# Performance work log

Measured on AMD Instinct MI355X. Metric: run time of the kernel, lower is better.

The kernel has to match this reference:

```python
import jax, jax.numpy as jnp
import numpy as np

N_OFFSETS = 72            # number of y-rows a lane proposal is sampled at (LaneATT)
N_STRIPS = N_OFFSETS - 1  # 71
IMG_W = 640.0             # nominal image width for x coordinates


def setup_inputs() -> dict:
    key = jax.random.key(0)
    k1, k2 = jax.random.split(key)
    n = 8192
    raw = jax.random.uniform(k1, (n, 2 + 3 + N_OFFSETS), dtype=jnp.float32)
    # LaneATT proposal layout: [score0, score1, start_y, start_x, length, xs(72)]
    start_y = raw[:, 2]                      # normalized [0,1]
    start_x = raw[:, 3] * IMG_W
    length = raw[:, 4] * N_STRIPS            # length in strips
    xs = raw[:, 5:] * IMG_W                  # x coords in pixels
    proposals = jnp.concatenate(
        [raw[:, :2], start_y[:, None], start_x[:, None], length[:, None], xs], axis=1
    )
    scores = jax.random.uniform(k2, (n,), dtype=jnp.float32)
    return {"proposals": proposals, "scores": scores, "nms_thres": 50, "nms_topk": 8}


def _line_nms(proposals, scores, nms_thres, nms_topk):
    """Greedy line NMS over lane proposals (LaneATT semantics)."""
    n = proposals.shape[0]
    order = jnp.argsort(-scores)
    p = proposals[order]                                   # [n, 77] sorted by score desc
    starts = jnp.round(p[:, 2] * N_STRIPS).astype(jnp.int32)       # [n]
    ends = jnp.minimum(starts + jnp.round(p[:, 4]).astype(jnp.int32) - 1, N_STRIPS)
    xs = p[:, 5:]                                          # [n, 72]
    k_idx = jnp.arange(N_OFFSETS)
    thr = jnp.float32(nms_thres)

    # suppression matrix row-by-row via lax.map to bound peak memory
    def supp_row(args):
        xi, si, ei = args
        ps = jnp.maximum(si, starts)                       # [n] pairwise overlap start
        pe = jnp.minimum(ei, ends)                         # [n] pairwise overlap end
        valid = (k_idx[None, :] >= ps[:, None]) & (k_idx[None, :] <= pe[:, None])
        d = jnp.sum(jnp.where(valid, jnp.abs(xi[None, :] - xs), 0.0), axis=1)
        cnt = jnp.maximum(pe - ps + 1, 1).astype(jnp.float32)
        return (pe >= ps) & (d / cnt < thr)                # [n] bool

    S = jax.lax.map(supp_row, (xs, starts, ends))          # [n, n] bool

    # sequential greedy pass: keep highest-score lane, suppress its neighbors
    def step(removed, inp):
        s_row, i = inp
        alive = ~removed[i]
        removed = removed | (alive & s_row)
        return removed, alive

    _, keep = jax.lax.scan(step, jnp.zeros((n,), bool), (S, jnp.arange(n)))

    rank = jnp.cumsum(keep)
    sel = keep & (rank <= nms_topk)
    idx = jnp.where(sel, size=nms_topk, fill_value=n)[0]   # padded with n (zero row)
    p_pad = jnp.concatenate([p, jnp.zeros((1, p.shape[1]), p.dtype)], axis=0)
    s_pad = jnp.concatenate([scores[order], jnp.zeros((1,), scores.dtype)], axis=0)
    kept = jnp.concatenate([p_pad[idx], s_pad[idx][:, None]], axis=1)  # [topk, 78]
    num_kept = jnp.minimum(jnp.sum(keep), nms_topk)
    return kept, num_kept


def reference(proposals, scores, nms_thres, nms_topk):
    return _line_nms(proposals, scores, nms_thres, nms_topk)
```

## Files before the change

### kernel.cpp

```cpp
#include <hip/hip_runtime.h>


#define NTH    256
#define SLOTS  32
#define NWAVES (NTH / 64)
#define N_OFF  72
#define NSTRIP 71
#define PROW   77
#define MAXK   8

__device__ __forceinline__ unsigned long long pack_key(float s, int idx) {
    return ((unsigned long long)__float_as_uint(s) << 32) |
           (unsigned long long)(0xFFFFFFFFu - (unsigned)idx);
}
__device__ __forceinline__ int key_idx(unsigned long long k) {
    return (int)(0xFFFFFFFFu - (unsigned)(k & 0xFFFFFFFFu));
}

__global__ __launch_bounds__(NTH, 1) void lane_nms(
    const float* __restrict__ prop,
    const float* __restrict__ scores,
    const int* __restrict__ p_thres,
    const int* __restrict__ p_topk,
    float* __restrict__ out,
    int n, int out_rows)
{
    const int tid  = threadIdx.x;
    const int lane = tid & 63;
    const int wv   = tid >> 6;

    __shared__ unsigned long long s_wmax[NWAVES];
    __shared__ float s_buf[2][PROW + 1];
    __shared__ float s_kxs[MAXK][N_OFF];
    __shared__ int   s_ks[MAXK], s_ke[MAXK];
    __shared__ int   s_sup[2];

    const float thr = (float)(*p_thres);
    int topk = *p_topk;
    if (topk > out_rows) topk = out_rows;
    if (topk > MAXK)     topk = MAXK;

    unsigned long long key[SLOTS];
#pragma unroll
    for (int jo = 0; jo < SLOTS / 4; ++jo) {
        int base = jo * (NTH * 4) + tid * 4;
        if (base + 3 < n) {
            const float4 s4 = *reinterpret_cast<const float4*>(scores + base);
            key[jo * 4 + 0] = pack_key(s4.x, base + 0);
            key[jo * 4 + 1] = pack_key(s4.y, base + 1);
            key[jo * 4 + 2] = pack_key(s4.z, base + 2);
            key[jo * 4 + 3] = pack_key(s4.w, base + 3);
        } else {
#pragma unroll
            for (int c = 0; c < 4; ++c) {
                int idx = base + c;
                key[jo * 4 + c] = (idx < n) ? pack_key(scores[idx], idx) : 0ULL;
            }
        }
    }
    if (tid == 0) { s_sup[0] = 0; s_sup[1] = 0; }

    auto scan = [&](unsigned long long lim) {
        unsigned long long m = 0ULL;
#pragma unroll
        for (int j = 0; j < SLOTS; ++j) {
            unsigned long long k = key[j];
            if (k < lim && k > m) m = k;
        }
#pragma unroll
        for (int off = 32; off > 0; off >>= 1) {
            unsigned long long o = __shfl_down(m, off);
            if (o > m) m = o;
        }
        if (lane == 0) s_wmax[wv] = m;
    };
    auto merge = [&]() {
        unsigned long long m = s_wmax[0];
#pragma unroll
        for (int i = 1; i < NWAVES; ++i)
            if (s_wmax[i] > m) m = s_wmax[i];
        return m;
    };

    scan(~0ULL);
    __syncthreads();
    unsigned long long k1 = merge();
    __syncthreads();
    scan(k1);
    __syncthreads();
    unsigned long long k2 = merge();

    if (k1 != 0ULL) {
        int w = key_idx(k1);
        if (tid < PROW)       s_buf[0][tid]  = prop[(size_t)w * PROW + tid];
        else if (tid == PROW) s_buf[0][PROW] = scores[w];
    }
    if (k2 != 0ULL) {
        int w = key_idx(k2);
        if (tid >= NTH - PROW - 1) {
            int t = tid - (NTH - PROW - 1);
            s_buf[1][t] = (t < PROW) ? prop[(size_t)w * PROW + t] : scores[w];
        }
    }
    __syncthreads();

    int kept = 0, p = 0, q = 0;
    unsigned long long curk = k1, nxtk = k2;

    if (topk > 0) {
        while (curk != 0ULL) {
            scan(nxtk);
            float sy = s_buf[p][2];
            float ln = s_buf[p][4];
            int cs = (int)rintf(sy * (float)NSTRIP);
            int ce = cs + (int)rintf(ln) - 1;
            if (ce > NSTRIP) ce = NSTRIP;
            if (tid < kept) {
                int ps = cs > s_ks[tid] ? cs : s_ks[tid];
                int pe = ce < s_ke[tid] ? ce : s_ke[tid];
                if (pe >= ps) {
                    float d = 0.0f;
                    for (int k = ps; k <= pe; ++k)
                        d += fabsf(s_buf[p][5 + k] - s_kxs[tid][k]);
                    if (d / (float)(pe - ps + 1) < thr) s_sup[q] = 1;
                }
            }
            if (tid == NTH - 1) s_sup[q ^ 1] = 0;
            __syncthreads();

            unsigned long long k3 = merge();
            if (s_sup[q] == 0) {
                if (tid < PROW + 1) out[kept * (PROW + 1) + tid] = s_buf[p][tid];
                if (tid < N_OFF)    s_kxs[kept][tid] = s_buf[p][5 + tid];
                if (tid == 0) { s_ks[kept] = cs; s_ke[kept] = ce; }
                ++kept;
                if (kept >= topk) break;
            }
            __syncthreads();

            if (k3 != 0ULL) {
                int w = key_idx(k3);
                if (tid < PROW)       s_buf[p][tid]  = prop[(size_t)w * PROW + tid];
                else if (tid == PROW) s_buf[p][PROW] = scores[w];
            }
            curk = nxtk; nxtk = k3; p ^= 1; q ^= 1;
        }
    }

    for (int i = tid; i < (out_rows - kept) * (PROW + 1); i += NTH)
        out[kept * (PROW + 1) + i] = 0.0f;
    if (tid == 0) out[out_rows * (PROW + 1)] = (float)kept;
}

extern "C" void kernel_launch(void* const* d_in, const int* in_sizes, int n_in,
                              void* d_out, int out_size, void* d_ws, size_t ws_size,
                              hipStream_t stream) {
    const float* prop   = (const float*)d_in[0];
    const float* scores = (const float*)d_in[1];
    const int*   thres  = (const int*)d_in[2];
    const int*   topk   = (const int*)d_in[3];
    int n        = in_sizes[1];
    int out_rows = (out_size - 1) / (PROW + 1);
    lane_nms<<<1, NTH, 0, stream>>>(prop, scores, thres, topk,
                                    (float*)d_out, n, out_rows);
}
```

Before: 87.26 us.

## Select top candidates via bitonic threshold and run greedy NMS in one wave

Replaces the per-step block-wide argmax scan with a one-time selection. Each thread takes its local max, a 64-lane bitonic sort of the per-thread maxima yields a threshold, and keys at or above it go into a small sorted candidate list. The first rows are prefetched into shared memory and a single wave runs the greedy suppression over the candidates with ballots, so the loop needs no block barriers. If the candidates run out before topk lanes are kept, it falls back to the original scan loop resuming below the last candidate, which adds code and shared memory.

```diff
diff --git a/kernel.cpp b/kernel.cpp
--- a/kernel.cpp
+++ b/kernel.cpp
@@ -1,13 +1,15 @@
 #include <hip/hip_runtime.h>
 
 
-#define NTH    256
-#define SLOTS  32
-#define NWAVES (NTH / 64)
-#define N_OFF  72
-#define NSTRIP 71
-#define PROW   77
-#define MAXK   8
+#define NTH     256
+#define SLOTS   32
+#define NWAVES  (NTH / 64)
+#define N_OFF   72
+#define NSTRIP  71
+#define PROW    77
+#define MAXK    8
+#define CANDMAX 64
+#define PRE     16
 
 __device__ __forceinline__ unsigned long long pack_key(float s, int idx) {
     return ((unsigned long long)__float_as_uint(s) << 32) |
@@ -15,6 +17,24 @@
 }
 __device__ __forceinline__ int key_idx(unsigned long long k) {
     return (int)(0xFFFFFFFFu - (unsigned)(k & 0xFFFFFFFFu));
+}
+
+__device__ __forceinline__ unsigned long long bitonic64_desc(
+        unsigned long long v, int lane) {
+#pragma unroll
+    for (int k = 2; k <= 64; k <<= 1) {
+#pragma unroll
+        for (int j = k >> 1; j > 0; j >>= 1) {
+            unsigned long long pv = __shfl_xor(v, j);
+            bool lower   = (lane & j) == 0;
+            bool dirdesc = (lane & k) != 0;
+            bool keepmax = (dirdesc != lower);
+            unsigned long long mx = v > pv ? v : pv;
+            unsigned long long mn = v > pv ? pv : v;
+            v = keepmax ? mx : mn;
+        }
+    }
+    return v;
 }
 
 __global__ __launch_bounds__(NTH, 1) void lane_nms(
@@ -30,10 +50,16 @@
     const int wv   = tid >> 6;
 
     __shared__ unsigned long long s_wmax[NWAVES];
+    __shared__ unsigned long long s_tmax[NTH];
+    __shared__ unsigned long long s_cand[CANDMAX];
+    __shared__ unsigned long long s_thr64;
+    __shared__ unsigned long long s_resume;
+    __shared__ float s_rows[PRE][PROW + 1];
     __shared__ float s_buf[2][PROW + 1];
     __shared__ float s_kxs[MAXK][N_OFF];
     __shared__ int   s_ks[MAXK], s_ke[MAXK];
     __shared__ int   s_sup[2];
+    __shared__ int   s_cnt, s_kept, s_fb;
 
     const float thr = (float)(*p_thres);
     int topk = *p_topk;
@@ -58,56 +84,167 @@
             }
         }
     }
-    if (tid == 0) { s_sup[0] = 0; s_sup[1] = 0; }
-
-    auto scan = [&](unsigned long long lim) {
-        unsigned long long m = 0ULL;
-#pragma unroll
-        for (int j = 0; j < SLOTS; ++j) {
-            unsigned long long k = key[j];
-            if (k < lim && k > m) m = k;
-        }
-#pragma unroll
-        for (int off = 32; off > 0; off >>= 1) {
-            unsigned long long o = __shfl_down(m, off);
-            if (o > m) m = o;
-        }
-        if (lane == 0) s_wmax[wv] = m;
-    };
-    auto merge = [&]() {
-        unsigned long long m = s_wmax[0];
-#pragma unroll
-        for (int i = 1; i < NWAVES; ++i)
-            if (s_wmax[i] > m) m = s_wmax[i];
-        return m;
-    };
-
-    scan(~0ULL);
+    unsigned long long tmax = 0ULL;
+#pragma unroll
+    for (int j = 0; j < SLOTS; ++j)
+        if (key[j] > tmax) tmax = key[j];
+
+    s_tmax[tid] = tmax;
+    if (tid == 0) { s_cnt = 0; s_sup[0] = 0; s_sup[1] = 0; }
     __syncthreads();
-    unsigned long long k1 = merge();
+
+    if (wv == 0) {
+        unsigned long long g = s_tmax[lane * 4 + 0];
+        unsigned long long t1 = s_tmax[lane * 4 + 1]; if (t1 > g) g = t1;
+        unsigned long long t2 = s_tmax[lane * 4 + 2]; if (t2 > g) g = t2;
+        unsigned long long t3 = s_tmax[lane * 4 + 3]; if (t3 > g) g = t3;
+        g = bitonic64_desc(g, lane);
+        if (lane == 15) s_thr64 = g;
+    }
     __syncthreads();
-    scan(k1);
+    const unsigned long long T = s_thr64;
+
+#pragma unroll
+    for (int j = 0; j < SLOTS; ++j) {
+        unsigned long long k = key[j];
+        if (k != 0ULL && k >= T) {
+            int pos = atomicAdd(&s_cnt, 1);
+            if (pos < CANDMAX) s_cand[pos] = k;
+        }
+    }
     __syncthreads();
-    unsigned long long k2 = merge();
-
-    if (k1 != 0ULL) {
-        int w = key_idx(k1);
-        if (tid < PROW)       s_buf[0][tid]  = prop[(size_t)w * PROW + tid];
-        else if (tid == PROW) s_buf[0][PROW] = scores[w];
-    }
-    if (k2 != 0ULL) {
-        int w = key_idx(k2);
-        if (tid >= NTH - PROW - 1) {
-            int t = tid - (NTH - PROW - 1);
-            s_buf[1][t] = (t < PROW) ? prop[(size_t)w * PROW + t] : scores[w];
-        }
-    }
-    __syncthreads();
-
-    int kept = 0, p = 0, q = 0;
-    unsigned long long curk = k1, nxtk = k2;
-
-    if (topk > 0) {
+    const int  cnt  = s_cnt;
+    const bool fast = (cnt <= CANDMAX) && (topk > 0);
+
+    int kept = 0;
+    bool fb = (topk > 0);
+    unsigned long long resume = ~0ULL;
+
+    if (fast) {
+        const int ncand = cnt;
+        if (wv == 0) {
+            unsigned long long v = (lane < ncand) ? s_cand[lane] : 0ULL;
+            v = bitonic64_desc(v, lane);
+            s_cand[lane] = v;
+        }
+        __syncthreads();
+
+        const int npre = ncand < PRE ? ncand : PRE;
+        for (int i = tid; i < npre * (PROW + 1); i += NTH) {
+            int r = i / (PROW + 1), c = i - r * (PROW + 1);
+            int w = key_idx(s_cand[r]);
+            s_rows[r][c] = (c < PROW) ? prop[(size_t)w * PROW + c] : scores[w];
+        }
+        __syncthreads();
+
+        if (wv == 0) {
+            int  pref = npre;
+            int  k0 = 0;
+            bool hit_topk = false;
+            for (int c = 0; c < ncand; ++c) {
+                if (c >= pref) {
+                    int w = key_idx(s_cand[c]);
+                    for (int i = lane; i < PROW + 1; i += 64)
+                        s_rows[c & (PRE - 1)][i] =
+                            (i < PROW) ? prop[(size_t)w * PROW + i] : scores[w];
+                    asm volatile("s_waitcnt lgkmcnt(0)" ::: "memory");
+                    pref = c + 1;
+                }
+                const int slot = c & (PRE - 1);
+                float sy = s_rows[slot][2];
+                float ln = s_rows[slot][4];
+                int cs = (int)rintf(sy * (float)NSTRIP);
+                int ce = cs + (int)rintf(ln) - 1;
+                if (ce > NSTRIP) ce = NSTRIP;
+
+                bool pred = false;
+                {
+                    int j = lane >> 3, l = lane & 7;
+                    if (j < k0) {
+                        int ps = cs > s_ks[j] ? cs : s_ks[j];
+                        int pe = ce < s_ke[j] ? ce : s_ke[j];
+                        if (pe >= ps) {
+                            float d = 0.0f;
+                            for (int k = ps + l; k <= pe; k += 8)
+                                d += fabsf(s_rows[slot][5 + k] - s_kxs[j][k]);
+                            d += __shfl_down(d, 4, 8);
+                            d += __shfl_down(d, 2, 8);
+                            d += __shfl_down(d, 1, 8);
+                            if (l == 0 && d / (float)(pe - ps + 1) < thr)
+                                pred = true;
+                        }
+                    }
+                }
+                if (__ballot((int)pred) == 0ULL) {
+                    for (int i = lane; i < PROW + 1; i += 64)
+                        out[k0 * (PROW + 1) + i] = s_rows[slot][i];
+                    for (int i = lane; i < N_OFF; i += 64)
+                        s_kxs[k0][i] = s_rows[slot][5 + i];
+                    if (lane == 0) { s_ks[k0] = cs; s_ke[k0] = ce; }
+                    ++k0;
+                    if (k0 >= topk) { hit_topk = true; break; }
+                    asm volatile("s_waitcnt lgkmcnt(0)" ::: "memory");
+                }
+            }
+            if (lane == 0) {
+                s_kept   = k0;
+                s_fb     = (!hit_topk && k0 < topk) ? 1 : 0;
+                s_resume = (ncand > 0) ? s_cand[ncand - 1] : 0ULL;
+            }
+        }
+        __syncthreads();
+        kept   = s_kept;
+        fb     = (s_fb != 0);
+        resume = s_resume;
+    }
+
+    if (fb && kept < topk) {
+        auto scan = [&](unsigned long long lim) {
+            unsigned long long m = 0ULL;
+#pragma unroll
+            for (int j = 0; j < SLOTS; ++j) {
+                unsigned long long k = key[j];
+                if (k < lim && k > m) m = k;
+            }
+#pragma unroll
+            for (int off = 32; off > 0; off >>= 1) {
+                unsigned long long o = __shfl_down(m, off);
+                if (o > m) m = o;
+            }
+            if (lane == 0) s_wmax[wv] = m;
+        };
+        auto merge = [&]() {
+            unsigned long long m = s_wmax[0];
+#pragma unroll
+            for (int i = 1; i < NWAVES; ++i)
+                if (s_wmax[i] > m) m = s_wmax[i];
+            return m;
+        };
+
+        scan(resume);
+        __syncthreads();
+        unsigned long long k1 = merge();
+        __syncthreads();
+        scan(k1);
+        __syncthreads();
+        unsigned long long k2 = merge();
+
+        if (k1 != 0ULL) {
+            int w = key_idx(k1);
+            if (tid < PROW)       s_buf[0][tid]  = prop[(size_t)w * PROW + tid];
+            else if (tid == PROW) s_buf[0][PROW] = scores[w];
+        }
+        if (k2 != 0ULL) {
+            int w = key_idx(k2);
+            if (tid >= NTH - PROW - 1) {
+                int t = tid - (NTH - PROW - 1);
+                s_buf[1][t] = (t < PROW) ? prop[(size_t)w * PROW + t] : scores[w];
+            }
+        }
+        __syncthreads();
+
+        int p = 0, q = 0;
+        unsigned long long curk = k1, nxtk = k2;
         while (curk != 0ULL) {
             scan(nxtk);
             float sy = s_buf[p][2];
```

Result: faster. 73.58 us (-15.7%).
